# Kernel tuning notes

Measured on AMD Instinct MI355X. Metric: run time of the kernel, lower is better.

The kernel has to match this reference:

```python
import jax, jax.numpy as jnp
import numpy as np

N_E = 8192
E_DIM = 512
N_TOK = 32768
EPS = 1e-10


def setup_inputs() -> dict:
    key = jax.random.key(0)
    k1, k2 = jax.random.split(key)
    z = jax.random.normal(k1, (N_TOK, E_DIM), dtype=jnp.float32)
    weight = jax.random.normal(k2, (N_E, E_DIM), dtype=jnp.float32)
    return {"z": z, "weight": weight}


def reference(z, weight):
    # d[n,k] = ||z_n||^2 + ||e_k||^2 - 2 z_n . e_k  -> [N, n_e]
    d = (jnp.sum(z ** 2, axis=1, keepdims=True)
         + jnp.sum(weight ** 2, axis=1)
         - 2.0 * jnp.matmul(z, weight.T))
    idx = jnp.argmin(d, axis=1)                      # [N]
    # gather instead of one-hot matmul (same math)
    z_q = jnp.take(weight, idx, axis=0)              # [N, e_dim]
    # straight-through estimator
    z_q = z + jax.lax.stop_gradient(z_q - z)
    # e_mean = mean of one-hot encodings = normalized histogram of idx
    counts = jnp.zeros((N_E,), dtype=z.dtype).at[idx].add(1.0)
    e_mean = counts / z.shape[0]
    perplexity = jnp.exp(-jnp.sum(e_mean * jnp.log(e_mean + EPS)))
    return (z_q, perplexity)
```

## Files before the change

kernel.cpp:

```cpp
#include <hip/hip_runtime.h>
#include <stdint.h>


#define NTOK 32768
#define NE   8192
#define DIM  512
#define MARGIN 16.0f

typedef __attribute__((ext_vector_type(8))) int   v8i;
typedef __attribute__((ext_vector_type(4))) int   v4i;
typedef __attribute__((ext_vector_type(4))) float f32x4;

#define SBAR   __builtin_amdgcn_s_barrier()
#define SCHED0 __builtin_amdgcn_sched_barrier(0)
#define SCALE1 0x7F7F7F7F

__device__ __forceinline__ void gl_lds16(const void* g, void* l) {
  __builtin_amdgcn_global_load_lds(
      (const __attribute__((address_space(1))) void*)g,
      (__attribute__((address_space(3))) void*)l, 16, 0, 0);
}

__device__ __forceinline__ int pk8(float a, float b, float c, float d) {
  int r = __builtin_amdgcn_cvt_pk_fp8_f32(a, b, 0, false);
  return __builtin_amdgcn_cvt_pk_fp8_f32(c, d, r, true);
}

__global__ void k_prep_z(const float* __restrict__ z, int2* __restrict__ zb) {
  int i = blockIdx.x * 256 + threadIdx.x;
  const float4* zp = (const float4*)z + (size_t)i * 2;
  float4 a = zp[0], b = zp[1];
  int2 o;
  o.x = pk8(-2.f * a.x, -2.f * a.y, -2.f * a.z, -2.f * a.w);
  o.y = pk8(-2.f * b.x, -2.f * b.y, -2.f * b.z, -2.f * b.w);
  zb[i] = o;
}

__global__ void k_prep_w(const float* __restrict__ w, int2* __restrict__ wb,
                         float* __restrict__ cnorm) {
  int row  = blockIdx.x * 4 + (threadIdx.x >> 6);
  int lane = threadIdx.x & 63;
  const float4* wp = (const float4*)(w + (size_t)row * DIM) + lane * 2;
  float4 a = wp[0], b = wp[1];
  int2 o;
  o.x = pk8(a.x, a.y, a.z, a.w);
  o.y = pk8(b.x, b.y, b.z, b.w);
  wb[(size_t)row * 64 + lane] = o;
  float s = a.x * a.x + a.y * a.y + a.z * a.z + a.w * a.w
          + b.x * b.x + b.y * b.y + b.z * b.z + b.w * b.w;
#pragma unroll
  for (int m = 1; m < 64; m <<= 1) s += __shfl_xor(s, m);
  if (lane == 0) cnorm[row] = s;
}

__global__ void __launch_bounds__(256) k_phase1(
    const unsigned char* __restrict__ zb, const unsigned char* __restrict__ wb,
    const float* __restrict__ cnorm, float* __restrict__ slot2,
    float* __restrict__ slot3) {
  __shared__ char S[2][32768];

  const int tid  = threadIdx.x;
  const int lane = tid & 63;
  const int wv   = tid >> 6;
  const int wr   = wv >> 1;
  const int wc   = wv & 1;
  const int swzb  = (blockIdx.x & 7) * 128 + (blockIdx.x >> 3);
  const int split = swzb >> 8;
  const int tb    = swzb & 255;
  const int l15  = lane & 15;

  const int srcsw = (((lane & 7) ^ ((lane >> 3) & 7)) << 4);
  const unsigned char* zsA = zb + (size_t)(tb * 128 + wv * 32 + (lane >> 3)) * 512 + srcsw;
  const unsigned char* zsB = wb + (size_t)(split * 2048 + wv * 32 + (lane >> 3)) * 512 + srcsw;

  const int offs0 = ((((lane >> 4) * 2) ^ (lane & 7)) << 4);
  const int offs1 = ((((lane >> 4) * 2 + 1) ^ (lane & 7)) << 4);
  int arow[4], brow[4];
#pragma unroll
  for (int i = 0; i < 4; ++i) {
    arow[i] = (wr * 64 + i * 16 + l15) * 128;
    brow[i] = 16384 + (wc * 64 + i * 16 + l15) * 128;
  }

  const float BIG = 3.0e38f;
  float m1s[4][4], m2s[4][4], m3s[4][4];
#pragma unroll
  for (int mi = 0; mi < 4; ++mi)
#pragma unroll
    for (int r = 0; r < 4; ++r) { m1s[mi][r] = BIG; m2s[mi][r] = BIG; m3s[mi][r] = BIG; }

  const unsigned int KMASK = 0xFFFFE000u;

  auto stage = [&](int g) {
    char* DA = &S[g & 1][wv * 4096];
    const unsigned char* ga = zsA + ((g & 3) << 7);
#pragma unroll
    for (int r = 0; r < 4; ++r) gl_lds16(ga + r * 4096, DA + r * 1024);
    char* DB = &S[g & 1][16384 + wv * 4096];
    const unsigned char* gb = zsB + ((size_t)(g >> 2) << 16) + ((g & 3) << 7);
#pragma unroll
    for (int r = 0; r < 4; ++r) gl_lds16(gb + r * 4096, DB + r * 1024);
  };

  stage(0);
  __syncthreads();

  for (int ct = 0; ct < 16; ++ct) {
    const int codebase = split * 2048 + ct * 128 + wc * 64 + l15;
    float cf0 = cnorm[codebase + 0];
    float cf1 = cnorm[codebase + 16];
    float cf2 = cnorm[codebase + 32];
    float cf3 = cnorm[codebase + 48];
    f32x4 acc[4][4];

#pragma unroll 1
    for (int kc = 0; kc < 4; ++kc) {
      const int g = ct * 4 + kc;
      if (g < 63) { stage(g + 1); asm volatile("s_waitcnt vmcnt(8)" ::: "memory"); }
      else        { asm volatile("s_waitcnt vmcnt(0)" ::: "memory"); }
      SBAR; SCHED0;
      const char* P = S[g & 1];
      v8i a[4], b[4];
#pragma unroll
      for (int i = 0; i < 4; ++i) {
        v4i alo = *(const v4i*)(P + arow[i] + offs0);
        v4i ahi = *(const v4i*)(P + arow[i] + offs1);
        a[i] = __builtin_shufflevector(alo, ahi, 0, 1, 2, 3, 4, 5, 6, 7);
        v4i blo = *(const v4i*)(P + brow[i] + offs0);
        v4i bhi = *(const v4i*)(P + brow[i] + offs1);
        b[i] = __builtin_shufflevector(blo, bhi, 0, 1, 2, 3, 4, 5, 6, 7);
      }
      __builtin_amdgcn_s_setprio(1);
      if (kc == 0) {
        f32x4 c0 = {cf0, cf0, cf0, cf0}, c1 = {cf1, cf1, cf1, cf1};
        f32x4 c2 = {cf2, cf2, cf2, cf2}, c3 = {cf3, cf3, cf3, cf3};
#pragma unroll
        for (int mi = 0; mi < 4; ++mi) {
          acc[mi][0] = __builtin_amdgcn_mfma_scale_f32_16x16x128_f8f6f4(a[mi], b[0], c0, 0, 0, 0, SCALE1, 0, SCALE1);
          acc[mi][1] = __builtin_amdgcn_mfma_scale_f32_16x16x128_f8f6f4(a[mi], b[1], c1, 0, 0, 0, SCALE1, 0, SCALE1);
          acc[mi][2] = __builtin_amdgcn_mfma_scale_f32_16x16x128_f8f6f4(a[mi], b[2], c2, 0, 0, 0, SCALE1, 0, SCALE1);
          acc[mi][3] = __builtin_amdgcn_mfma_scale_f32_16x16x128_f8f6f4(a[mi], b[3], c3, 0, 0, 0, SCALE1, 0, SCALE1);
        }
      } else {
#pragma unroll
        for (int mi = 0; mi < 4; ++mi)
#pragma unroll
          for (int fj = 0; fj < 4; ++fj)
            acc[mi][fj] = __builtin_amdgcn_mfma_scale_f32_16x16x128_f8f6f4(a[mi], b[fj], acc[mi][fj], 0, 0, 0, SCALE1, 0, SCALE1);
      }
      __builtin_amdgcn_s_setprio(0);
      SBAR;
    }

#pragma unroll
    for (int mi = 0; mi < 4; ++mi) {
#pragma unroll
      for (int r = 0; r < 4; ++r) {
        float M1 = m1s[mi][r], M2 = m2s[mi][r], M3 = m3s[mi][r];
#pragma unroll
        for (int fj = 0; fj < 4; ++fj) {
          float kf = __uint_as_float((__float_as_uint(acc[mi][fj][r]) & KMASK) |
                                     (unsigned)(codebase + fj * 16));
          float t3 = fminf(M3, fmaxf(M2, kf));
          float t2 = fminf(M2, fmaxf(M1, kf));
          M1 = fminf(M1, kf); M2 = t2; M3 = t3;
        }
        m1s[mi][r] = M1; m2s[mi][r] = M2; m3s[mi][r] = M3;
      }
    }
  }

  const int cell = split * 32 + wc * 16 + l15;
#pragma unroll
  for (int mi = 0; mi < 4; ++mi) {
#pragma unroll
    for (int r = 0; r < 4; ++r) {
      int token = tb * 128 + wr * 64 + mi * 16 + (lane >> 4) * 4 + r;
      ((float2*)(slot2 + (size_t)token * 256))[cell] = make_float2(m1s[mi][r], m2s[mi][r]);
      slot3[(size_t)token * 128 + cell] = m3s[mi][r];
    }
  }
}

__global__ void k_select(const float* __restrict__ slot2, const float* __restrict__ slot3,
                         const float* __restrict__ z, const float* __restrict__ w,
                         unsigned int* __restrict__ counts, float* __restrict__ out) {
  const int lane = threadIdx.x & 63;
  const int t = blockIdx.x * 4 + (threadIdx.x >> 6);

  float4 e = *(const float4*)(slot2 + (size_t)t * 256 + lane * 4);
  float2 q = *(const float2*)(slot3 + (size_t)t * 128 + lane * 2);
  float pk = fminf(e.x, e.z);
#pragma unroll
  for (int m = 1; m < 64; m <<= 1) pk = fminf(pk, __shfl_xor(pk, m));
  const unsigned int mb = __float_as_uint(pk);
  int best = (int)(mb & 0x1FFFu);
  const float thr = __uint_as_float(mb & 0xFFFFE000u) + MARGIN;

  const unsigned int KM = 0xFFFFE000u;
  bool c0 = __uint_as_float(__float_as_uint(e.x) & KM) < thr;
  bool c1 = __uint_as_float(__float_as_uint(e.y) & KM) < thr;
  bool c2 = __uint_as_float(__float_as_uint(e.z) & KM) < thr;
  bool c3 = __uint_as_float(__float_as_uint(e.w) & KM) < thr;
  bool h0 = __uint_as_float(__float_as_uint(q.x) & KM) < thr;
  bool h1 = __uint_as_float(__float_as_uint(q.y) & KM) < thr;
  unsigned long long B0 = __ballot(c0), B1 = __ballot(c1);
  unsigned long long B2 = __ballot(c2), B3 = __ballot(c3);
  unsigned long long H0 = __ballot(h0), H1 = __ballot(h1);
  int nc = __popcll(B0) + __popcll(B1) + __popcll(B2) + __popcll(B3);

  if (nc > 1) {
    const float4* zp = (const float4*)(z + (size_t)t * DIM) + lane * 2;
    float4 za = zp[0], zc = zp[1];
    double bestd = 1e300;
    int besti = NE;

    auto eval = [&](int code) {
      const float4* wp = (const float4*)(w + (size_t)code * DIM) + lane * 2;
      float4 wa = wp[0], wv2 = wp[1];
      double d = (double)wa.x * ((double)wa.x - 2.0 * (double)za.x)
               + (double)wa.y * ((double)wa.y - 2.0 * (double)za.y)
               + (double)wa.z * ((double)wa.z - 2.0 * (double)za.z)
               + (double)wa.w * ((double)wa.w - 2.0 * (double)za.w)
               + (double)wv2.x * ((double)wv2.x - 2.0 * (double)zc.x)
               + (double)wv2.y * ((double)wv2.y - 2.0 * (double)zc.y)
               + (double)wv2.z * ((double)wv2.z - 2.0 * (double)zc.z)
               + (double)wv2.w * ((double)wv2.w - 2.0 * (double)zc.w);
#pragma unroll
      for (int m = 1; m < 64; m <<= 1) d += __shfl_xor(d, m);
      if (d < bestd || (d == bestd && code < besti)) { bestd = d; besti = code; }
    };
    auto scan_cell = [&](int cid) {
      int sp = cid >> 5, wcc = (cid >> 4) & 1, col = cid & 15;
      int base = sp * 2048 + wcc * 64 + col;
      for (int ctt = 0; ctt < 16; ++ctt)
        for (int nf = 0; nf < 4; ++nf)
          eval(base + ctt * 128 + nf * 16);
    };

    int i0 = (int)(__float_as_uint(e.x) & 0x1FFFu);
    int i1 = (int)(__float_as_uint(e.y) & 0x1FFFu);
    int i2 = (int)(__float_as_uint(e.z) & 0x1FFFu);
    int i3 = (int)(__float_as_uint(e.w) & 0x1FFFu);
    unsigned long long bm;
    bm = __ballot(c0 && !h0); while (bm) { int s = __ffsll(bm) - 1; bm &= bm - 1; eval(__shfl(i0, s)); }
    bm = __ballot(c1 && !h0); while (bm) { int s = __ffsll(bm) - 1; bm &= bm - 1; eval(__shfl(i1, s)); }
    bm = __ballot(c2 && !h1); while (bm) { int s = __ffsll(bm) - 1; bm &= bm - 1; eval(__shfl(i2, s)); }
    bm = __ballot(c3 && !h1); while (bm) { int s = __ffsll(bm) - 1; bm &= bm - 1; eval(__shfl(i3, s)); }
    bm = H0; while (bm) { int s = __ffsll(bm) - 1; bm &= bm - 1; scan_cell(2 * s); }
    bm = H1; while (bm) { int s = __ffsll(bm) - 1; bm &= bm - 1; scan_cell(2 * s + 1); }
    best = besti;
  }
  if (lane == 0) atomicAdd(&counts[best], 1u);
  const float4* wr4 = (const float4*)(w + (size_t)best * DIM);
  float4* o4 = (float4*)(out + (size_t)t * DIM);
  o4[lane]      = wr4[lane];
  o4[lane + 64] = wr4[lane + 64];
}

__global__ void k_perp(const unsigned int* __restrict__ counts, float* __restrict__ out) {
  __shared__ float red[16];
  float s = 0.f;
  for (int k = threadIdx.x; k < NE; k += 1024) {
    float p = (float)counts[k] * (1.0f / (float)NTOK);
    s += p * logf(p + 1e-10f);
  }
#pragma unroll
  for (int m = 1; m < 64; m <<= 1) s += __shfl_xor(s, m);
  int lane = threadIdx.x & 63, wv = threadIdx.x >> 6;
  if (lane == 0) red[wv] = s;
  __syncthreads();
  if (threadIdx.x == 0) {
    float tot = 0.f;
    for (int i = 0; i < 16; ++i) tot += red[i];
    out[(size_t)NTOK * DIM] = expf(-tot);
  }
}

extern "C" void kernel_launch(void* const* d_in, const int* in_sizes, int n_in,
                              void* d_out, int out_size, void* d_ws, size_t ws_size,
                              hipStream_t stream) {
  const float* z = (const float*)d_in[0];
  const float* w = (const float*)d_in[1];
  float* out = (float*)d_out;
  char* ws = (char*)d_ws;

  unsigned char* zb     = (unsigned char*)(ws);
  float*        slot3   = (float*)(ws + 16777216);
  unsigned char* wb     = (unsigned char*)(ws + 33554432);
  float*        cnorm   = (float*)(ws + 41943040);
  float*        slot2   = (float*)(ws + 41975808);
  unsigned int* counts  = (unsigned int*)(ws + 75661312);

  k_prep_z<<<8192, 256, 0, stream>>>(z, (int2*)zb);
  k_prep_w<<<2048, 256, 0, stream>>>(w, (int2*)wb, cnorm);
  k_phase1<<<1024, 256, 0, stream>>>(zb, wb, cnorm, slot2, slot3);
  hipMemsetAsync(counts, 0, NE * sizeof(unsigned int), stream);
  k_select<<<8192, 256, 0, stream>>>(slot2, slot3, z, w, counts, out);
  k_perp<<<1, 1024, 0, stream>>>(counts, out);
}
```

Before: 277.8 us.

## Enlarge phase1 GEMM tile to 256x256 with 8 waves per block

The FP8 distance GEMM block tile grows from 128x128 to 256x256, with 512 threads and 128 KB of double-buffered LDS. Each wave now covers 64 tokens by 128 codes and processes its B fragments in two halves of four. The select kernel's cell-scan indexing is updated to match the new code-to-cell mapping. The aim is higher arithmetic intensity and fewer global loads per MFMA, at the cost of more accumulator registers, lower occupancy, and fewer blocks in flight.

```diff
diff --git a/kernel.cpp b/kernel.cpp
--- a/kernel.cpp
+++ b/kernel.cpp
@@ -53,34 +53,33 @@
   if (lane == 0) cnorm[row] = s;
 }
 
-__global__ void __launch_bounds__(256) k_phase1(
+__global__ void __launch_bounds__(512) k_phase1(
     const unsigned char* __restrict__ zb, const unsigned char* __restrict__ wb,
     const float* __restrict__ cnorm, float* __restrict__ slot2,
     float* __restrict__ slot3) {
-  __shared__ char S[2][32768];
+  __shared__ char S[2][65536];
 
   const int tid  = threadIdx.x;
   const int lane = tid & 63;
   const int wv   = tid >> 6;
-  const int wr   = wv >> 1;
-  const int wc   = wv & 1;
-  const int swzb  = (blockIdx.x & 7) * 128 + (blockIdx.x >> 3);
-  const int split = swzb >> 8;
-  const int tb    = swzb & 255;
+  const int wrM  = wv >> 1;
+  const int wcN  = wv & 1;
+  const int swzb  = (blockIdx.x & 7) * 64 + (blockIdx.x >> 3);
+  const int split = swzb >> 7;
+  const int tb    = swzb & 127;
   const int l15  = lane & 15;
 
   const int srcsw = (((lane & 7) ^ ((lane >> 3) & 7)) << 4);
-  const unsigned char* zsA = zb + (size_t)(tb * 128 + wv * 32 + (lane >> 3)) * 512 + srcsw;
+  const unsigned char* zsA = zb + (size_t)(tb * 256 + wv * 32 + (lane >> 3)) * 512 + srcsw;
   const unsigned char* zsB = wb + (size_t)(split * 2048 + wv * 32 + (lane >> 3)) * 512 + srcsw;
 
   const int offs0 = ((((lane >> 4) * 2) ^ (lane & 7)) << 4);
   const int offs1 = ((((lane >> 4) * 2 + 1) ^ (lane & 7)) << 4);
-  int arow[4], brow[4];
-#pragma unroll
-  for (int i = 0; i < 4; ++i) {
-    arow[i] = (wr * 64 + i * 16 + l15) * 128;
-    brow[i] = 16384 + (wc * 64 + i * 16 + l15) * 128;
-  }
+  int arow[4], brow[8];
+#pragma unroll
+  for (int i = 0; i < 4; ++i) arow[i] = (wrM * 64 + i * 16 + l15) * 128;
+#pragma unroll
+  for (int j = 0; j < 8; ++j) brow[j] = 32768 + (wcN * 128 + j * 16 + l15) * 128;
 
   const float BIG = 3.0e38f;
   float m1s[4][4], m2s[4][4], m3s[4][4];
@@ -92,63 +91,91 @@
   const unsigned int KMASK = 0xFFFFE000u;
 
   auto stage = [&](int g) {
-    char* DA = &S[g & 1][wv * 4096];
+    char* base = S[g & 1];
     const unsigned char* ga = zsA + ((g & 3) << 7);
 #pragma unroll
-    for (int r = 0; r < 4; ++r) gl_lds16(ga + r * 4096, DA + r * 1024);
-    char* DB = &S[g & 1][16384 + wv * 4096];
-    const unsigned char* gb = zsB + ((size_t)(g >> 2) << 16) + ((g & 3) << 7);
-#pragma unroll
-    for (int r = 0; r < 4; ++r) gl_lds16(gb + r * 4096, DB + r * 1024);
+    for (int r = 0; r < 4; ++r) gl_lds16(ga + r * 4096, base + wv * 4096 + r * 1024);
+    const unsigned char* gb = zsB + ((size_t)(g >> 2) << 17) + ((g & 3) << 7);
+#pragma unroll
+    for (int r = 0; r < 4; ++r) gl_lds16(gb + r * 4096, base + 32768 + wv * 4096 + r * 1024);
   };
 
   stage(0);
   __syncthreads();
 
-  for (int ct = 0; ct < 16; ++ct) {
-    const int codebase = split * 2048 + ct * 128 + wc * 64 + l15;
-    float cf0 = cnorm[codebase + 0];
-    float cf1 = cnorm[codebase + 16];
-    float cf2 = cnorm[codebase + 32];
-    float cf3 = cnorm[codebase + 48];
-    f32x4 acc[4][4];
+  for (int ct = 0; ct < 8; ++ct) {
+    const int codebase = split * 2048 + ct * 256 + wcN * 128 + l15;
+    float cf[8];
+#pragma unroll
+    for (int j = 0; j < 8; ++j) cf[j] = cnorm[codebase + j * 16];
+    f32x4 acc[4][8];
 
 #pragma unroll 1
     for (int kc = 0; kc < 4; ++kc) {
       const int g = ct * 4 + kc;
-      if (g < 63) { stage(g + 1); asm volatile("s_waitcnt vmcnt(8)" ::: "memory"); }
+      if (g < 31) { stage(g + 1); asm volatile("s_waitcnt vmcnt(8)" ::: "memory"); }
       else        { asm volatile("s_waitcnt vmcnt(0)" ::: "memory"); }
       SBAR; SCHED0;
       const char* P = S[g & 1];
-      v8i a[4], b[4];
+      v8i a[4];
 #pragma unroll
       for (int i = 0; i < 4; ++i) {
-        v4i alo = *(const v4i*)(P + arow[i] + offs0);
-        v4i ahi = *(const v4i*)(P + arow[i] + offs1);
-        a[i] = __builtin_shufflevector(alo, ahi, 0, 1, 2, 3, 4, 5, 6, 7);
-        v4i blo = *(const v4i*)(P + brow[i] + offs0);
-        v4i bhi = *(const v4i*)(P + brow[i] + offs1);
-        b[i] = __builtin_shufflevector(blo, bhi, 0, 1, 2, 3, 4, 5, 6, 7);
+        v4i lo = *(const v4i*)(P + arow[i] + offs0);
+        v4i hi = *(const v4i*)(P + arow[i] + offs1);
+        a[i] = __builtin_shufflevector(lo, hi, 0, 1, 2, 3, 4, 5, 6, 7);
       }
-      __builtin_amdgcn_s_setprio(1);
-      if (kc == 0) {
-        f32x4 c0 = {cf0, cf0, cf0, cf0}, c1 = {cf1, cf1, cf1, cf1};
-        f32x4 c2 = {cf2, cf2, cf2, cf2}, c3 = {cf3, cf3, cf3, cf3};
-#pragma unroll
-        for (int mi = 0; mi < 4; ++mi) {
-          acc[mi][0] = __builtin_amdgcn_mfma_scale_f32_16x16x128_f8f6f4(a[mi], b[0], c0, 0, 0, 0, SCALE1, 0, SCALE1);
-          acc[mi][1] = __builtin_amdgcn_mfma_scale_f32_16x16x128_f8f6f4(a[mi], b[1], c1, 0, 0, 0, SCALE1, 0, SCALE1);
-          acc[mi][2] = __builtin_amdgcn_mfma_scale_f32_16x16x128_f8f6f4(a[mi], b[2], c2, 0, 0, 0, SCALE1, 0, SCALE1);
-          acc[mi][3] = __builtin_amdgcn_mfma_scale_f32_16x16x128_f8f6f4(a[mi], b[3], c3, 0, 0, 0, SCALE1, 0, SCALE1);
-        }
-      } else {
-#pragma unroll
-        for (int mi = 0; mi < 4; ++mi)
-#pragma unroll
-          for (int fj = 0; fj < 4; ++fj)
-            acc[mi][fj] = __builtin_amdgcn_mfma_scale_f32_16x16x128_f8f6f4(a[mi], b[fj], acc[mi][fj], 0, 0, 0, SCALE1, 0, SCALE1);
+      {
+        v8i b[4];
+#pragma unroll
+        for (int j = 0; j < 4; ++j) {
+          v4i lo = *(const v4i*)(P + brow[j] + offs0);
+          v4i hi = *(const v4i*)(P + brow[j] + offs1);
+          b[j] = __builtin_shufflevector(lo, hi, 0, 1, 2, 3, 4, 5, 6, 7);
+        }
+        __builtin_amdgcn_s_setprio(1);
+        if (kc == 0) {
+#pragma unroll
+          for (int mi = 0; mi < 4; ++mi)
+#pragma unroll
+            for (int j = 0; j < 4; ++j) {
+              f32x4 c = {cf[j], cf[j], cf[j], cf[j]};
+              acc[mi][j] = __builtin_amdgcn_mfma_scale_f32_16x16x128_f8f6f4(a[mi], b[j], c, 0, 0, 0, SCALE1, 0, SCALE1);
+            }
+        } else {
+#pragma unroll
+          for (int mi = 0; mi < 4; ++mi)
+#pragma unroll
+            for (int j = 0; j < 4; ++j)
+              acc[mi][j] = __builtin_amdgcn_mfma_scale_f32_16x16x128_f8f6f4(a[mi], b[j], acc[mi][j], 0, 0, 0, SCALE1, 0, SCALE1);
+        }
+        __builtin_amdgcn_s_setprio(0);
       }
-      __builtin_amdgcn_s_setprio(0);
+      {
+        v8i b[4];
+#pragma unroll
+        for (int j = 0; j < 4; ++j) {
+          v4i lo = *(const v4i*)(P + brow[j + 4] + offs0);
+          v4i hi = *(const v4i*)(P + brow[j + 4] + offs1);
+          b[j] = __builtin_shufflevector(lo, hi, 0, 1, 2, 3, 4, 5, 6, 7);
+        }
+        __builtin_amdgcn_s_setprio(1);
+        if (kc == 0) {
+#pragma unroll
+          for (int mi = 0; mi < 4; ++mi)
+#pragma unroll
+            for (int j = 0; j < 4; ++j) {
+              f32x4 c = {cf[j + 4], cf[j + 4], cf[j + 4], cf[j + 4]};
+              acc[mi][j + 4] = __builtin_amdgcn_mfma_scale_f32_16x16x128_f8f6f4(a[mi], b[j], c, 0, 0, 0, SCALE1, 0, SCALE1);
+            }
+        } else {
+#pragma unroll
+          for (int mi = 0; mi < 4; ++mi)
+#pragma unroll
+            for (int j = 0; j < 4; ++j)
+              acc[mi][j + 4] = __builtin_amdgcn_mfma_scale_f32_16x16x128_f8f6f4(a[mi], b[j], acc[mi][j + 4], 0, 0, 0, SCALE1, 0, SCALE1);
+        }
+        __builtin_amdgcn_s_setprio(0);
+      }
       SBAR;
     }
 
@@ -158,9 +185,9 @@
       for (int r = 0; r < 4; ++r) {
         float M1 = m1s[mi][r], M2 = m2s[mi][r], M3 = m3s[mi][r];
 #pragma unroll
-        for (int fj = 0; fj < 4; ++fj) {
-          float kf = __uint_as_float((__float_as_uint(acc[mi][fj][r]) & KMASK) |
-                                     (unsigned)(codebase + fj * 16));
+        for (int j = 0; j < 8; ++j) {
+          float kf = __uint_as_float((__float_as_uint(acc[mi][j][r]) & KMASK) |
+                                     (unsigned)(codebase + j * 16));
           float t3 = fminf(M3, fmaxf(M2, kf));
           float t2 = fminf(M2, fmaxf(M1, kf));
           M1 = fminf(M1, kf); M2 = t2; M3 = t3;
@@ -170,12 +197,12 @@
     }
   }
 
-  const int cell = split * 32 + wc * 16 + l15;
+  const int cell = split * 32 + wcN * 16 + l15;
 #pragma unroll
   for (int mi = 0; mi < 4; ++mi) {
 #pragma unroll
     for (int r = 0; r < 4; ++r) {
-      int token = tb * 128 + wr * 64 + mi * 16 + (lane >> 4) * 4 + r;
+      int token = tb * 256 + wrM * 64 + mi * 16 + (lane >> 4) * 4 + r;
       ((float2*)(slot2 + (size_t)token * 256))[cell] = make_float2(m1s[mi][r], m2s[mi][r]);
       slot3[(size_t)token * 128 + cell] = m3s[mi][r];
     }
@@ -232,10 +259,10 @@
     };
     auto scan_cell = [&](int cid) {
       int sp = cid >> 5, wcc = (cid >> 4) & 1, col = cid & 15;
-      int base = sp * 2048 + wcc * 64 + col;
-      for (int ctt = 0; ctt < 16; ++ctt)
-        for (int nf = 0; nf < 4; ++nf)
-          eval(base + ctt * 128 + nf * 16);
+      int base = sp * 2048 + wcc * 128 + col;
+      for (int ctt = 0; ctt < 8; ++ctt)
+        for (int fj = 0; fj < 8; ++fj)
+          eval(base + ctt * 256 + fj * 16);
     };
 
     int i0 = (int)(__float_as_uint(e.x) & 0x1FFFu);
@@ -294,7 +321,7 @@
 
   k_prep_z<<<8192, 256, 0, stream>>>(z, (int2*)zb);
   k_prep_w<<<2048, 256, 0, stream>>>(w, (int2*)wb, cnorm);
-  k_phase1<<<1024, 256, 0, stream>>>(zb, wb, cnorm, slot2, slot3);
+  k_phase1<<<512, 512, 0, stream>>>(zb, wb, cnorm, slot2, slot3);
   hipMemsetAsync(counts, 0, NE * sizeof(unsigned int), stream);
   k_select<<<8192, 256, 0, stream>>>(slot2, slot3, z, w, counts, out);
   k_perp<<<1, 1024, 0, stream>>>(counts, out);
```

After: 382.0 us. 1.37x slower.
